# Optimization experiments

Hardware: AMD Instinct MI355X
Metric: run time of the kernel (lower is better)

## Reference

```python
import jax, jax.numpy as jnp
import numpy as np

N_NODES = 50000
N_EDGES = 800000
F_IN = 128
HEADS = 8
HID = 16
EDGE_DIM = 2
EPS = 1e-5
GAT_SLOPE = 0.2   # GATv2Conv default negative_slope
ACT_SLOPE = 0.01  # GATLayer alpha


def setup_inputs() -> dict:
    key = jax.random.key(0)
    ks = jax.random.split(key, 10)
    HC = HEADS * HID
    return {
        "x": jax.random.normal(ks[0], (N_NODES, F_IN), jnp.float32),
        "edge_idx": jax.random.randint(ks[1], (2, N_EDGES), 0, N_NODES, jnp.int32),
        "edge_attr": jax.random.normal(ks[2], (N_EDGES, EDGE_DIM), jnp.float32),
        "Wl": jax.random.normal(ks[3], (F_IN, HC), jnp.float32) * (1.0 / np.sqrt(F_IN)),
        "bl": jnp.zeros((HC,), jnp.float32),
        "Wr": jax.random.normal(ks[4], (F_IN, HC), jnp.float32) * (1.0 / np.sqrt(F_IN)),
        "br": jnp.zeros((HC,), jnp.float32),
        "We": jax.random.normal(ks[5], (EDGE_DIM, HC), jnp.float32) * (1.0 / np.sqrt(EDGE_DIM)),
        "be": jnp.zeros((HC,), jnp.float32),
        "att": jax.random.normal(ks[6], (HEADS, HID), jnp.float32) * (1.0 / np.sqrt(HID)),
        "bias": jnp.zeros((HC,), jnp.float32),
        "gamma": jnp.ones((HC,), jnp.float32),
        "beta": jnp.zeros((HC,), jnp.float32),
    }


def reference(x, edge_idx, edge_attr, Wl, bl, Wr, br, We, be, att, bias, gamma, beta):
    N = x.shape[0]
    H, C = att.shape
    # GATv2: separate source/target linear maps (share_weights=False)
    xl = (x @ Wl + bl).reshape(N, H, C)      # source transform (messages)
    xr = (x @ Wr + br).reshape(N, H, C)      # target transform
    e = (edge_attr @ We + be).reshape(-1, H, C)
    src, dst = edge_idx[0], edge_idx[1]       # edge j -> i
    # edge-wise attention input: [E, H, C]
    m = jax.nn.leaky_relu(xl[src] + xr[dst] + e, GAT_SLOPE)
    logits = jnp.einsum('ehc,hc->eh', m, att)  # [E, H]
    # segment softmax over incoming edges of each target node
    lmax = jax.ops.segment_max(logits, dst, num_segments=N)          # [N, H]
    ex = jnp.exp(logits - lmax[dst])
    denom = jax.ops.segment_sum(ex, dst, num_segments=N)             # [N, H]
    alpha = ex / denom[dst]                                          # [E, H]
    # weighted scatter-aggregate of source messages, concat heads
    out = jax.ops.segment_sum(xl[src] * alpha[:, :, None], dst, num_segments=N)
    out = out.reshape(N, H * C) + bias
    # BatchNorm over nodes (batch statistics), then LeakyReLU(0.01)
    mean = out.mean(axis=0)
    var = out.var(axis=0)
    out = (out - mean) / jnp.sqrt(var + EPS) * gamma + beta
    return jax.nn.leaky_relu(out, ACT_SLOPE)
```

## Files before the change

kernel.cpp:

```cpp
#include <hip/hip_runtime.h>
#include <hip/hip_bf16.h>

#define N_NODES 50000
#define N_EDGES 800000
#define HEADS 8
#define HID 16
#define HC 128

typedef __attribute__((ext_vector_type(8))) short bf16x8;
typedef __attribute__((ext_vector_type(4))) float f32x4;

__device__ __forceinline__ float bf2f(unsigned short u) {
  union { unsigned int i; float f; } v;
  v.i = (unsigned int)u << 16;
  return v.f;
}
__device__ __forceinline__ unsigned short f2bf(float f) {
  __hip_bfloat16 h = __float2bfloat16(f);
  return *(unsigned short*)&h;
}

__global__ __launch_bounds__(256) void k_cvt_x(const float* __restrict__ x,
                                               unsigned short* __restrict__ xb) {
  const int i = blockIdx.x * 256 + threadIdx.x;
  const float4 a = ((const float4*)x)[(size_t)i * 2];
  const float4 b = ((const float4*)x)[(size_t)i * 2 + 1];
  union { unsigned short s[8]; uint4 v; } o;
  o.s[0] = f2bf(a.x); o.s[1] = f2bf(a.y); o.s[2] = f2bf(a.z); o.s[3] = f2bf(a.w);
  o.s[4] = f2bf(b.x); o.s[5] = f2bf(b.y); o.s[6] = f2bf(b.z); o.s[7] = f2bf(b.w);
  ((uint4*)xb)[i] = o.v;
}

__global__ __launch_bounds__(128) void k_cvt_w(const float* __restrict__ Wl,
                                               const float* __restrict__ Wr,
                                               unsigned short* __restrict__ WcatT) {
  const int n = blockIdx.x;
  const int k = threadIdx.x;
  const float* W = (n < 128) ? Wl : Wr;
  WcatT[n * 128 + k] = f2bf(W[k * HC + (n & 127)]);
}

__global__ __launch_bounds__(256) void k_gemm(
    const unsigned short* __restrict__ xb, const unsigned short* __restrict__ WcatT,
    const float* __restrict__ bl, const float* __restrict__ br,
    unsigned short* __restrict__ xl, unsigned short* __restrict__ xr) {
  __shared__ unsigned short As[128 * 136];
  const int t = threadIdx.x;
  const int m0 = blockIdx.x * 128;
  const int nt = blockIdx.y;

#pragma unroll
  for (int it = 0; it < 8; ++it) {
    const int c = t + it * 256;
    const int row = c >> 4, c8 = (c & 15) * 8;
    uint4 v = make_uint4(0, 0, 0, 0);
    if (m0 + row < N_NODES) v = *(const uint4*)(xb + (size_t)(m0 + row) * HC + c8);
    *(uint4*)(&As[row * 136 + c8]) = v;
  }
  __syncthreads();

  const int w = t >> 6, lane = t & 63;
  const int wm = w >> 1, wn = w & 1;
  const int lr = lane & 15, lk = lane >> 4;

  f32x4 acc[4][4];
#pragma unroll
  for (int i = 0; i < 4; ++i)
#pragma unroll
    for (int j = 0; j < 4; ++j) acc[i][j] = (f32x4)(0.f);

  const unsigned short* Wbase = WcatT + (size_t)(nt * 128 + wn * 64 + lr) * 128;
#pragma unroll
  for (int ks = 0; ks < 4; ++ks) {
    const int k = ks * 32 + lk * 8;
    bf16x8 bfr[4], afr[4];
#pragma unroll
    for (int ni = 0; ni < 4; ++ni)
      bfr[ni] = *(const bf16x8*)(Wbase + ni * 16 * 128 + k);
#pragma unroll
    for (int mi = 0; mi < 4; ++mi)
      afr[mi] = *(const bf16x8*)(&As[(wm * 64 + mi * 16 + lr) * 136 + k]);
#pragma unroll
    for (int mi = 0; mi < 4; ++mi)
#pragma unroll
      for (int ni = 0; ni < 4; ++ni)
        acc[mi][ni] = __builtin_amdgcn_mfma_f32_16x16x32_bf16(
            afr[mi], bfr[ni], acc[mi][ni], 0, 0, 0);
  }

  const float* bvec = nt ? br : bl;
  unsigned short* __restrict__ dst = nt ? xr : xl;
#pragma unroll
  for (int ni = 0; ni < 4; ++ni) {
    const int gcol = wn * 64 + ni * 16 + lr;
    const float bb = bvec[gcol];
#pragma unroll
    for (int mi = 0; mi < 4; ++mi) {
#pragma unroll
      for (int r = 0; r < 4; ++r) {
        const int grow = m0 + wm * 64 + mi * 16 + lk * 4 + r;
        if (grow < N_NODES)
          dst[(size_t)grow * HC + gcol] = f2bf(acc[mi][ni][r] + bb);
      }
    }
  }
}

__global__ __launch_bounds__(256) void k_deg(const int* __restrict__ eidx,
                                             int* __restrict__ deg) {
  const int e = blockIdx.x * 256 + threadIdx.x;
  if (e < N_EDGES) atomicAdd(&deg[eidx[N_EDGES + e]], 1);
}

__global__ __launch_bounds__(256) void k_alloc(const int* __restrict__ deg,
                                               int* __restrict__ counter,
                                               int* __restrict__ offs) {
  const int node = blockIdx.x * 256 + threadIdx.x;
  const int lane = threadIdx.x & 63;
  const int v = (node < N_NODES) ? deg[node] : 0;
  int incl = v;
#pragma unroll
  for (int d = 1; d < 64; d <<= 1) {
    const int t = __shfl_up(incl, d);
    if (lane >= d) incl += t;
  }
  const int total = __shfl(incl, 63);
  int base = 0;
  if (lane == 63) base = atomicAdd(counter, total);
  base = __shfl(base, 63);
  if (node < N_NODES) offs[node] = base + incl - v;
}

__global__ __launch_bounds__(256) void k_scatter(
    const int* __restrict__ eidx, const float* __restrict__ eattr,
    const int* __restrict__ offs, int* __restrict__ cursor,
    int4* __restrict__ epack) {
  const int e = blockIdx.x * 256 + threadIdx.x;
  if (e < N_EDGES) {
    const int src = eidx[e];
    const int d = eidx[N_EDGES + e];
    const float2 ea = *(const float2*)(eattr + (size_t)e * 2);
    const int pos = atomicAdd(&cursor[d], 1);
    epack[offs[d] + pos] =
        make_int4(src, __float_as_int(ea.x), __float_as_int(ea.y), 0);
  }
}

__global__ __launch_bounds__(256) void k_attagg(
    const int* __restrict__ offs, const int* __restrict__ deg,
    const int4* __restrict__ epack,
    const unsigned short* __restrict__ xl, const unsigned short* __restrict__ xr,
    const float* __restrict__ We, const float* __restrict__ be,
    const float* __restrict__ att, float* __restrict__ outp) {
  const int wave = threadIdx.x >> 6, lane = threadIdx.x & 63;
  const int node = blockIdx.x * 4 + wave;
  const int c0 = lane * 2;

  const float w0a = We[c0],      w0b = We[c0 + 1];
  const float w1a = We[HC + c0], w1b = We[HC + c0 + 1];
  const float bea = be[c0],      beb = be[c0 + 1];
  const float ata = att[c0],     atb = att[c0 + 1];

  const unsigned int xrw = *((const unsigned int*)(xr + (size_t)node * HC) + lane);
  const float xra = bf2f((unsigned short)xrw);
  const float xrb = bf2f((unsigned short)(xrw >> 16));

  const int beg = offs[node];
  const int end = beg + deg[node];
  float dn = 0.f, a0 = 0.f, a1 = 0.f;

  if (beg < end) {
    const int endm1 = end - 1;
    const int nb = (end - beg + 3) >> 2;
    int4 ep0[4], ep1[4];
    unsigned int xw0[4];
#pragma unroll
    for (int j = 0; j < 4; ++j) {
      int kk = beg + j; kk = kk < endm1 ? kk : endm1;
      ep0[j] = epack[kk];
    }
#pragma unroll
    for (int j = 0; j < 4; ++j)
      xw0[j] = *((const unsigned int*)(xl + (size_t)ep0[j].x * HC) + lane);
    if (nb > 1) {
#pragma unroll
      for (int j = 0; j < 4; ++j) {
        int kk = beg + 4 + j; kk = kk < endm1 ? kk : endm1;
        ep1[j] = epack[kk];
      }
    }
    for (int b = 0; b < nb; ++b) {
      unsigned int xw1[4];
      int4 ep2[4];
      if (b + 1 < nb) {
#pragma unroll
        for (int j = 0; j < 4; ++j)
          xw1[j] = *((const unsigned int*)(xl + (size_t)ep1[j].x * HC) + lane);
      }
      if (b + 2 < nb) {
#pragma unroll
        for (int j = 0; j < 4; ++j) {
          int kk = beg + (b + 2) * 4 + j; kk = kk < endm1 ? kk : endm1;
          ep2[j] = epack[kk];
        }
      }
      const int k0 = beg + b * 4;
#pragma unroll
      for (int j = 0; j < 4; ++j) {
        const float eax = __int_as_float(ep0[j].y);
        const float eay = __int_as_float(ep0[j].z);
        const float x0 = bf2f((unsigned short)xw0[j]);
        const float x1 = bf2f((unsigned short)(xw0[j] >> 16));
        float m0 = x0 + xra + fmaf(eax, w0a, fmaf(eay, w1a, bea));
        float m1 = x1 + xrb + fmaf(eax, w0b, fmaf(eay, w1b, beb));
        m0 = m0 > 0.f ? m0 : 0.2f * m0;
        m1 = m1 > 0.f ? m1 : 0.2f * m1;
        float p = fmaf(m0, ata, m1 * atb);
        p += __shfl_xor(p, 1);
        p += __shfl_xor(p, 2);
        p += __shfl_xor(p, 4);
        const float exv = (k0 + j < end) ? __expf(p) : 0.f;
        dn += exv;
        a0 = fmaf(exv, x0, a0);
        a1 = fmaf(exv, x1, a1);
      }
#pragma unroll
      for (int j = 0; j < 4; ++j) { ep0[j] = ep1[j]; xw0[j] = xw1[j]; ep1[j] = ep2[j]; }
    }
  }
  const float inv = dn > 0.f ? 1.0f / dn : 0.f;
  float2 o;
  o.x = a0 * inv;
  o.y = a1 * inv;
  *((float2*)(outp + (size_t)node * HC) + lane) = o;
}

__global__ __launch_bounds__(256) void k_stats(const float* __restrict__ outp,
                                               float* __restrict__ stats) {
  const int c = threadIdx.x & 127;
  const int half = threadIdx.x >> 7;
  float s1 = 0.f, s2 = 0.f;
  for (int r = blockIdx.x * 2 + half; r < N_NODES; r += gridDim.x * 2) {
    const float v = outp[(size_t)r * HC + c];
    s1 += v;
    s2 = fmaf(v, v, s2);
  }
  __shared__ float sm[512];
  sm[threadIdx.x] = s1;
  sm[256 + threadIdx.x] = s2;
  __syncthreads();
  if (threadIdx.x < 128) {
    s1 = sm[threadIdx.x] + sm[threadIdx.x + 128];
    s2 = sm[256 + threadIdx.x] + sm[256 + threadIdx.x + 128];
    atomicAdd(&stats[c], s1);
    atomicAdd(&stats[128 + c], s2);
  }
}

__global__ __launch_bounds__(256) void k_bn(const float* __restrict__ stats,
                                            const float* __restrict__ gamma,
                                            const float* __restrict__ beta,
                                            float* __restrict__ outp) {
  const int i = blockIdx.x * 256 + threadIdx.x;
  if (i >= N_NODES * HC) return;
  const int c = i & 127;
  const float mean = stats[c] * (1.0f / N_NODES);
  const float var = stats[128 + c] * (1.0f / N_NODES) - mean * mean;
  const float rstd = rsqrtf(var + 1e-5f);
  float v = (outp[i] - mean) * rstd * gamma[c] + beta[c];
  outp[i] = v > 0.f ? v : 0.01f * v;
}

extern "C" void kernel_launch(void* const* d_in, const int* in_sizes, int n_in,
                              void* d_out, int out_size, void* d_ws, size_t ws_size,
                              hipStream_t stream) {
  const float* x     = (const float*)d_in[0];
  const int*   eidx  = (const int*)d_in[1];
  const float* eattr = (const float*)d_in[2];
  const float* Wl    = (const float*)d_in[3];
  const float* bl    = (const float*)d_in[4];
  const float* Wr    = (const float*)d_in[5];
  const float* br    = (const float*)d_in[6];
  const float* We    = (const float*)d_in[7];
  const float* be    = (const float*)d_in[8];
  const float* att   = (const float*)d_in[9];
  const float* gamma = (const float*)d_in[11];
  const float* beta  = (const float*)d_in[12];
  float* out = (float*)d_out;

  char* ws = (char*)d_ws;
  size_t off = 0;
  auto alloc = [&](size_t bytes) {
    size_t o = off;
    off = (off + bytes + 15) & ~size_t(15);
    return o;
  };
  const size_t o_deg   = alloc((size_t)(N_NODES + 1) * 4);
  const size_t o_cur   = alloc((size_t)N_NODES * 4);
  const size_t o_cnt   = alloc(16);
  const size_t o_stats = alloc(256 * 4);
  const size_t zero_bytes = off;
  const size_t o_offs = alloc((size_t)(N_NODES + 1) * 4);
  const size_t o_ep   = alloc((size_t)N_EDGES * 16);
  const size_t o_xb   = alloc((size_t)N_NODES * HC * 2);
  const size_t o_wt   = alloc((size_t)256 * 128 * 2);
  const size_t o_xl   = alloc((size_t)N_NODES * HC * 2);
  const size_t o_xr   = alloc((size_t)N_NODES * HC * 2);
  (void)ws_size; (void)in_sizes; (void)n_in; (void)out_size;

  int*   deg   = (int*)(ws + o_deg);
  int*   cur   = (int*)(ws + o_cur);
  int*   cnt   = (int*)(ws + o_cnt);
  float* stats = (float*)(ws + o_stats);
  int*   offs  = (int*)(ws + o_offs);
  int4*  epack = (int4*)(ws + o_ep);
  unsigned short* xb    = (unsigned short*)(ws + o_xb);
  unsigned short* WcatT = (unsigned short*)(ws + o_wt);
  unsigned short* xl    = (unsigned short*)(ws + o_xl);
  unsigned short* xr    = (unsigned short*)(ws + o_xr);

  hipMemsetAsync(ws, 0, zero_bytes, stream);

  k_cvt_x<<<3125, 256, 0, stream>>>(x, xb);
  k_cvt_w<<<256, 128, 0, stream>>>(Wl, Wr, WcatT);
  k_gemm<<<dim3(391, 2), 256, 0, stream>>>(xb, WcatT, bl, br, xl, xr);
  k_deg<<<3125, 256, 0, stream>>>(eidx, deg);
  k_alloc<<<196, 256, 0, stream>>>(deg, cnt, offs);
  k_scatter<<<3125, 256, 0, stream>>>(eidx, eattr, offs, cur, epack);
  k_attagg<<<12500, 256, 0, stream>>>(offs, deg, epack, xl, xr, We, be, att, out);
  k_stats<<<256, 256, 0, stream>>>(out, stats);
  k_bn<<<25000, 256, 0, stream>>>(stats, gamma, beta, out);
}
```

Measured before the change: 346.9 us.

## Fuse prep kernels, fold x conversion into GEMM, fuse BN stats into aggregation

Merges the degree count and weight transpose into one launch. The x-to-bf16 conversion moves into a single GEMM launch that computes both xl and xr per tile, and the offset allocation runs as extra blocks of that same launch. BatchNorm statistics are accumulated inside the attention/aggregation kernel into 8 bucketed atomics, which removes a separate stats pass over the output. The BN apply is vectorised with precomputed scale and shift, and the edge loop drops its clamped tail handling in favour of a separate remainder loop. Together these cut launches and full-tensor passes, at the cost of more atomics and more shared-memory work per aggregation block.

```diff
diff --git a/kernel.cpp b/kernel.cpp
--- a/kernel.cpp
+++ b/kernel.cpp
@@ -20,47 +20,73 @@
   return *(unsigned short*)&h;
 }
 
-__global__ __launch_bounds__(256) void k_cvt_x(const float* __restrict__ x,
-                                               unsigned short* __restrict__ xb) {
-  const int i = blockIdx.x * 256 + threadIdx.x;
-  const float4 a = ((const float4*)x)[(size_t)i * 2];
-  const float4 b = ((const float4*)x)[(size_t)i * 2 + 1];
-  union { unsigned short s[8]; uint4 v; } o;
-  o.s[0] = f2bf(a.x); o.s[1] = f2bf(a.y); o.s[2] = f2bf(a.z); o.s[3] = f2bf(a.w);
-  o.s[4] = f2bf(b.x); o.s[5] = f2bf(b.y); o.s[6] = f2bf(b.z); o.s[7] = f2bf(b.w);
-  ((uint4*)xb)[i] = o.v;
-}
-
-__global__ __launch_bounds__(128) void k_cvt_w(const float* __restrict__ Wl,
-                                               const float* __restrict__ Wr,
-                                               unsigned short* __restrict__ WcatT) {
-  const int n = blockIdx.x;
-  const int k = threadIdx.x;
-  const float* W = (n < 128) ? Wl : Wr;
-  WcatT[n * 128 + k] = f2bf(W[k * HC + (n & 127)]);
-}
-
-__global__ __launch_bounds__(256) void k_gemm(
-    const unsigned short* __restrict__ xb, const unsigned short* __restrict__ WcatT,
+__global__ __launch_bounds__(256) void k_prep(
+    const int* __restrict__ eidx, const float* __restrict__ Wl,
+    const float* __restrict__ Wr, int* __restrict__ deg,
+    unsigned short* __restrict__ WcatT) {
+  const int b = blockIdx.x;
+  if (b < 3125) {
+    const int e = b * 256 + threadIdx.x;
+    atomicAdd(&deg[eidx[N_EDGES + e]], 1);
+  } else {
+    const int idx = (b - 3125) * 256 + threadIdx.x;
+    const int n = idx >> 7, k = idx & 127;
+    const float* W = (n < 128) ? Wl : Wr;
+    WcatT[idx] = f2bf(W[k * HC + (n & 127)]);
+  }
+}
+
+__global__ __launch_bounds__(512) void k_gemm_alloc(
+    const float* __restrict__ x, const unsigned short* __restrict__ WcatT,
     const float* __restrict__ bl, const float* __restrict__ br,
-    unsigned short* __restrict__ xl, unsigned short* __restrict__ xr) {
+    unsigned short* __restrict__ xl, unsigned short* __restrict__ xr,
+    const int* __restrict__ deg, int* __restrict__ counter,
+    int* __restrict__ offs) {
   __shared__ unsigned short As[128 * 136];
   const int t = threadIdx.x;
+
+  if (blockIdx.x >= 391) {
+    const int node = (blockIdx.x - 391) * 512 + t;
+    const int lane = t & 63;
+    const int v = (node < N_NODES) ? deg[node] : 0;
+    int incl = v;
+#pragma unroll
+    for (int d = 1; d < 64; d <<= 1) {
+      const int tt = __shfl_up(incl, d);
+      if (lane >= d) incl += tt;
+    }
+    const int total = __shfl(incl, 63);
+    int base = 0;
+    if (lane == 63) base = atomicAdd(counter, total);
+    base = __shfl(base, 63);
+    if (node < N_NODES) offs[node] = base + incl - v;
+    return;
+  }
+
   const int m0 = blockIdx.x * 128;
-  const int nt = blockIdx.y;
-
-#pragma unroll
-  for (int it = 0; it < 8; ++it) {
-    const int c = t + it * 256;
-    const int row = c >> 4, c8 = (c & 15) * 8;
-    uint4 v = make_uint4(0, 0, 0, 0);
-    if (m0 + row < N_NODES) v = *(const uint4*)(xb + (size_t)(m0 + row) * HC + c8);
-    *(uint4*)(&As[row * 136 + c8]) = v;
+#pragma unroll
+  for (int it = 0; it < 4; ++it) {
+    const int c = t + it * 512;
+    const int row = c >> 4;
+    const int seg = (c & 15) * 8;
+    const int grow = m0 + row;
+    float4 a = make_float4(0.f, 0.f, 0.f, 0.f), bb2 = a;
+    if (grow < N_NODES) {
+      const float4* p = (const float4*)(x + (size_t)grow * 128 + seg);
+      a = p[0];
+      bb2 = p[1];
+    }
+    union { unsigned short s[8]; uint4 v; } o;
+    o.s[0] = f2bf(a.x);   o.s[1] = f2bf(a.y);
+    o.s[2] = f2bf(a.z);   o.s[3] = f2bf(a.w);
+    o.s[4] = f2bf(bb2.x); o.s[5] = f2bf(bb2.y);
+    o.s[6] = f2bf(bb2.z); o.s[7] = f2bf(bb2.w);
+    *(uint4*)(&As[row * 136 + seg]) = o.v;
   }
   __syncthreads();
 
   const int w = t >> 6, lane = t & 63;
-  const int wm = w >> 1, wn = w & 1;
+  const int wm = w >> 2, wn = w & 3;
   const int lr = lane & 15, lk = lane >> 4;
 
   f32x4 acc[4][4];
@@ -69,7 +95,7 @@
 #pragma unroll
     for (int j = 0; j < 4; ++j) acc[i][j] = (f32x4)(0.f);
 
-  const unsigned short* Wbase = WcatT + (size_t)(nt * 128 + wn * 64 + lr) * 128;
+  const unsigned short* Wbase = WcatT + (size_t)(wn * 64 + lr) * 128;
 #pragma unroll
   for (int ks = 0; ks < 4; ++ks) {
     const int k = ks * 32 + lk * 8;
@@ -88,47 +114,22 @@
             afr[mi], bfr[ni], acc[mi][ni], 0, 0, 0);
   }
 
-  const float* bvec = nt ? br : bl;
-  unsigned short* __restrict__ dst = nt ? xr : xl;
 #pragma unroll
   for (int ni = 0; ni < 4; ++ni) {
     const int gcol = wn * 64 + ni * 16 + lr;
-    const float bb = bvec[gcol];
+    const bool left = gcol < 128;
+    const float bb = left ? bl[gcol] : br[gcol - 128];
+    unsigned short* __restrict__ dst = left ? xl : xr;
+    const int cc = gcol & 127;
 #pragma unroll
     for (int mi = 0; mi < 4; ++mi) {
 #pragma unroll
       for (int r = 0; r < 4; ++r) {
         const int grow = m0 + wm * 64 + mi * 16 + lk * 4 + r;
-        if (grow < N_NODES)
-          dst[(size_t)grow * HC + gcol] = f2bf(acc[mi][ni][r] + bb);
+        if (grow < N_NODES) dst[(size_t)grow * HC + cc] = f2bf(acc[mi][ni][r] + bb);
       }
     }
   }
-}
-
-__global__ __launch_bounds__(256) void k_deg(const int* __restrict__ eidx,
-                                             int* __restrict__ deg) {
-  const int e = blockIdx.x * 256 + threadIdx.x;
-  if (e < N_EDGES) atomicAdd(&deg[eidx[N_EDGES + e]], 1);
-}
-
-__global__ __launch_bounds__(256) void k_alloc(const int* __restrict__ deg,
-                                               int* __restrict__ counter,
-                                               int* __restrict__ offs) {
-  const int node = blockIdx.x * 256 + threadIdx.x;
-  const int lane = threadIdx.x & 63;
-  const int v = (node < N_NODES) ? deg[node] : 0;
-  int incl = v;
-#pragma unroll
-  for (int d = 1; d < 64; d <<= 1) {
-    const int t = __shfl_up(incl, d);
-    if (lane >= d) incl += t;
-  }
-  const int total = __shfl(incl, 63);
-  int base = 0;
-  if (lane == 63) base = atomicAdd(counter, total);
-  base = __shfl(base, 63);
-  if (node < N_NODES) offs[node] = base + incl - v;
 }
 
 __global__ __launch_bounds__(256) void k_scatter(
@@ -136,139 +137,146 @@
     const int* __restrict__ offs, int* __restrict__ cursor,
     int4* __restrict__ epack) {
   const int e = blockIdx.x * 256 + threadIdx.x;
-  if (e < N_EDGES) {
-    const int src = eidx[e];
-    const int d = eidx[N_EDGES + e];
-    const float2 ea = *(const float2*)(eattr + (size_t)e * 2);
-    const int pos = atomicAdd(&cursor[d], 1);
-    epack[offs[d] + pos] =
-        make_int4(src, __float_as_int(ea.x), __float_as_int(ea.y), 0);
-  }
-}
+  const int src = eidx[e];
+  const int d = eidx[N_EDGES + e];
+  const float2 ea = *(const float2*)(eattr + (size_t)e * 2);
+  const int pos = atomicAdd(&cursor[d], 1);
+  epack[offs[d] + pos] = make_int4(src, __float_as_int(ea.x), __float_as_int(ea.y), 0);
+}
+
+#define LOADB(EP, K)                                   \
+  _Pragma("unroll") for (int j = 0; j < 4; ++j) EP[j] = epack[(K) + j];
+#define LOADX(XW, EP)                                  \
+  _Pragma("unroll") for (int j = 0; j < 4; ++j)        \
+      XW[j] = *((const unsigned int*)(xl + (size_t)EP[j].x * HC) + lane);
+#define EDGE1(EPJ, XWJ)                                                     \
+  {                                                                         \
+    const float eax = __int_as_float((EPJ).y);                              \
+    const float eay = __int_as_float((EPJ).z);                              \
+    const float x0 = bf2f((unsigned short)(XWJ));                           \
+    const float x1 = bf2f((unsigned short)((XWJ) >> 16));                   \
+    float m0 = fmaf(eax, w0a, fmaf(eay, w1a, ca)) + x0;                     \
+    float m1 = fmaf(eax, w0b, fmaf(eay, w1b, cb)) + x1;                     \
+    m0 = fmaxf(m0, 0.2f * m0);                                              \
+    m1 = fmaxf(m1, 0.2f * m1);                                              \
+    float p = fmaf(m0, ata, m1 * atb);                                      \
+    p += __shfl_xor(p, 1);                                                  \
+    p += __shfl_xor(p, 2);                                                  \
+    p += __shfl_xor(p, 4);                                                  \
+    const float exv = __expf(p);                                            \
+    dn += exv;                                                              \
+    a0 = fmaf(exv, x0, a0);                                                 \
+    a1 = fmaf(exv, x1, a1);                                                 \
+  }
+#define COMPUTE4(EP, XW)                               \
+  _Pragma("unroll") for (int j = 0; j < 4; ++j) EDGE1(EP[j], XW[j])
 
 __global__ __launch_bounds__(256) void k_attagg(
     const int* __restrict__ offs, const int* __restrict__ deg,
     const int4* __restrict__ epack,
     const unsigned short* __restrict__ xl, const unsigned short* __restrict__ xr,
     const float* __restrict__ We, const float* __restrict__ be,
-    const float* __restrict__ att, float* __restrict__ outp) {
+    const float* __restrict__ att, float* __restrict__ outp,
+    float* __restrict__ statsB) {
+  __shared__ float ssum[4 * 128];
+  __shared__ float ssq[4 * 128];
   const int wave = threadIdx.x >> 6, lane = threadIdx.x & 63;
   const int node = blockIdx.x * 4 + wave;
   const int c0 = lane * 2;
 
   const float w0a = We[c0],      w0b = We[c0 + 1];
   const float w1a = We[HC + c0], w1b = We[HC + c0 + 1];
-  const float bea = be[c0],      beb = be[c0 + 1];
   const float ata = att[c0],     atb = att[c0 + 1];
 
   const unsigned int xrw = *((const unsigned int*)(xr + (size_t)node * HC) + lane);
-  const float xra = bf2f((unsigned short)xrw);
-  const float xrb = bf2f((unsigned short)(xrw >> 16));
+  const float ca = be[c0] + bf2f((unsigned short)xrw);
+  const float cb = be[c0 + 1] + bf2f((unsigned short)(xrw >> 16));
 
   const int beg = offs[node];
-  const int end = beg + deg[node];
+  const int dn_e = deg[node];
+  const int end = beg + dn_e;
+  const int nf = dn_e >> 2;
+
   float dn = 0.f, a0 = 0.f, a1 = 0.f;
 
-  if (beg < end) {
-    const int endm1 = end - 1;
-    const int nb = (end - beg + 3) >> 2;
-    int4 ep0[4], ep1[4];
-    unsigned int xw0[4];
-#pragma unroll
-    for (int j = 0; j < 4; ++j) {
-      int kk = beg + j; kk = kk < endm1 ? kk : endm1;
-      ep0[j] = epack[kk];
-    }
-#pragma unroll
-    for (int j = 0; j < 4; ++j)
-      xw0[j] = *((const unsigned int*)(xl + (size_t)ep0[j].x * HC) + lane);
-    if (nb > 1) {
-#pragma unroll
-      for (int j = 0; j < 4; ++j) {
-        int kk = beg + 4 + j; kk = kk < endm1 ? kk : endm1;
-        ep1[j] = epack[kk];
-      }
-    }
-    for (int b = 0; b < nb; ++b) {
-      unsigned int xw1[4];
-      int4 ep2[4];
-      if (b + 1 < nb) {
-#pragma unroll
-        for (int j = 0; j < 4; ++j)
-          xw1[j] = *((const unsigned int*)(xl + (size_t)ep1[j].x * HC) + lane);
-      }
-      if (b + 2 < nb) {
-#pragma unroll
-        for (int j = 0; j < 4; ++j) {
-          int kk = beg + (b + 2) * 4 + j; kk = kk < endm1 ? kk : endm1;
-          ep2[j] = epack[kk];
-        }
-      }
-      const int k0 = beg + b * 4;
-#pragma unroll
-      for (int j = 0; j < 4; ++j) {
-        const float eax = __int_as_float(ep0[j].y);
-        const float eay = __int_as_float(ep0[j].z);
-        const float x0 = bf2f((unsigned short)xw0[j]);
-        const float x1 = bf2f((unsigned short)(xw0[j] >> 16));
-        float m0 = x0 + xra + fmaf(eax, w0a, fmaf(eay, w1a, bea));
-        float m1 = x1 + xrb + fmaf(eax, w0b, fmaf(eay, w1b, beb));
-        m0 = m0 > 0.f ? m0 : 0.2f * m0;
-        m1 = m1 > 0.f ? m1 : 0.2f * m1;
-        float p = fmaf(m0, ata, m1 * atb);
-        p += __shfl_xor(p, 1);
-        p += __shfl_xor(p, 2);
-        p += __shfl_xor(p, 4);
-        const float exv = (k0 + j < end) ? __expf(p) : 0.f;
-        dn += exv;
-        a0 = fmaf(exv, x0, a0);
-        a1 = fmaf(exv, x1, a1);
-      }
-#pragma unroll
-      for (int j = 0; j < 4; ++j) { ep0[j] = ep1[j]; xw0[j] = xw1[j]; ep1[j] = ep2[j]; }
-    }
-  }
+  if (nf >= 1) {
+    int4 epA[4], epB[4];
+    unsigned int xwA[4];
+    LOADB(epA, beg)
+    LOADX(xwA, epA)
+    if (nf >= 2) LOADB(epB, beg + 4)
+    for (int b = 0; b + 1 < nf; ++b) {
+      unsigned int xwB[4];
+      int4 epC[4];
+      LOADX(xwB, epB)
+      if (b + 2 < nf) LOADB(epC, beg + (b + 2) * 4)
+      COMPUTE4(epA, xwA)
+#pragma unroll
+      for (int j = 0; j < 4; ++j) { epA[j] = epB[j]; xwA[j] = xwB[j]; epB[j] = epC[j]; }
+    }
+    COMPUTE4(epA, xwA)
+  }
+  for (int k = beg + (nf << 2); k < end; ++k) {
+    const int4 ep = epack[k];
+    const unsigned int xw = *((const unsigned int*)(xl + (size_t)ep.x * HC) + lane);
+    EDGE1(ep, xw)
+  }
+
   const float inv = dn > 0.f ? 1.0f / dn : 0.f;
+  const float o0 = a0 * inv, o1 = a1 * inv;
   float2 o;
-  o.x = a0 * inv;
-  o.y = a1 * inv;
+  o.x = o0;
+  o.y = o1;
   *((float2*)(outp + (size_t)node * HC) + lane) = o;
-}
-
-__global__ __launch_bounds__(256) void k_stats(const float* __restrict__ outp,
-                                               float* __restrict__ stats) {
-  const int c = threadIdx.x & 127;
-  const int half = threadIdx.x >> 7;
-  float s1 = 0.f, s2 = 0.f;
-  for (int r = blockIdx.x * 2 + half; r < N_NODES; r += gridDim.x * 2) {
-    const float v = outp[(size_t)r * HC + c];
-    s1 += v;
-    s2 = fmaf(v, v, s2);
-  }
-  __shared__ float sm[512];
-  sm[threadIdx.x] = s1;
-  sm[256 + threadIdx.x] = s2;
+
+  ssum[wave * 128 + c0]     = o0;
+  ssum[wave * 128 + c0 + 1] = o1;
+  ssq[wave * 128 + c0]      = o0 * o0;
+  ssq[wave * 128 + c0 + 1]  = o1 * o1;
   __syncthreads();
   if (threadIdx.x < 128) {
-    s1 = sm[threadIdx.x] + sm[threadIdx.x + 128];
-    s2 = sm[256 + threadIdx.x] + sm[256 + threadIdx.x + 128];
-    atomicAdd(&stats[c], s1);
-    atomicAdd(&stats[128 + c], s2);
-  }
-}
-
-__global__ __launch_bounds__(256) void k_bn(const float* __restrict__ stats,
+    const int c = threadIdx.x;
+    const float s1 = ssum[c] + ssum[128 + c] + ssum[256 + c] + ssum[384 + c];
+    const float s2 = ssq[c] + ssq[128 + c] + ssq[256 + c] + ssq[384 + c];
+    float* bkt = statsB + (blockIdx.x & 7) * 256;
+    atomicAdd(&bkt[c], s1);
+    atomicAdd(&bkt[128 + c], s2);
+  }
+}
+
+__global__ __launch_bounds__(256) void k_bn(const float* __restrict__ statsB,
                                             const float* __restrict__ gamma,
                                             const float* __restrict__ beta,
                                             float* __restrict__ outp) {
-  const int i = blockIdx.x * 256 + threadIdx.x;
-  if (i >= N_NODES * HC) return;
-  const int c = i & 127;
-  const float mean = stats[c] * (1.0f / N_NODES);
-  const float var = stats[128 + c] * (1.0f / N_NODES) - mean * mean;
-  const float rstd = rsqrtf(var + 1e-5f);
-  float v = (outp[i] - mean) * rstd * gamma[c] + beta[c];
-  outp[i] = v > 0.f ? v : 0.01f * v;
+  __shared__ float sscale[128], sshift[128];
+  const int t = threadIdx.x;
+  if (t < 128) {
+    float s1 = 0.f, s2 = 0.f;
+#pragma unroll
+    for (int b = 0; b < 8; ++b) {
+      s1 += statsB[b * 256 + t];
+      s2 += statsB[b * 256 + 128 + t];
+    }
+    const float mean = s1 * (1.0f / N_NODES);
+    const float var = s2 * (1.0f / N_NODES) - mean * mean;
+    const float rstd = rsqrtf(var + 1e-5f);
+    const float sc = rstd * gamma[t];
+    sscale[t] = sc;
+    sshift[t] = beta[t] - mean * sc;
+  }
+  __syncthreads();
+  const size_t base = (size_t)blockIdx.x * 1024 + t * 4;
+  float4 v = *(const float4*)(outp + base);
+  const int c = (t * 4) & 127;
+  v.x = fmaf(v.x, sscale[c],     sshift[c]);
+  v.y = fmaf(v.y, sscale[c + 1], sshift[c + 1]);
+  v.z = fmaf(v.z, sscale[c + 2], sshift[c + 2]);
+  v.w = fmaf(v.w, sscale[c + 3], sshift[c + 3]);
+  v.x = fmaxf(v.x, 0.01f * v.x);
+  v.y = fmaxf(v.y, 0.01f * v.y);
+  v.z = fmaxf(v.z, 0.01f * v.z);
+  v.w = fmaxf(v.w, 0.01f * v.w);
+  *(float4*)(outp + base) = v;
 }
 
 extern "C" void kernel_launch(void* const* d_in, const int* in_sizes, int n_in,
@@ -298,36 +306,31 @@
   const size_t o_deg   = alloc((size_t)(N_NODES + 1) * 4);
   const size_t o_cur   = alloc((size_t)N_NODES * 4);
   const size_t o_cnt   = alloc(16);
-  const size_t o_stats = alloc(256 * 4);
+  const size_t o_stats = alloc((size_t)8 * 256 * 4);
   const size_t zero_bytes = off;
   const size_t o_offs = alloc((size_t)(N_NODES + 1) * 4);
   const size_t o_ep   = alloc((size_t)N_EDGES * 16);
-  const size_t o_xb   = alloc((size_t)N_NODES * HC * 2);
   const size_t o_wt   = alloc((size_t)256 * 128 * 2);
   const size_t o_xl   = alloc((size_t)N_NODES * HC * 2);
   const size_t o_xr   = alloc((size_t)N_NODES * HC * 2);
   (void)ws_size; (void)in_sizes; (void)n_in; (void)out_size;
 
-  int*   deg   = (int*)(ws + o_deg);
-  int*   cur   = (int*)(ws + o_cur);
-  int*   cnt   = (int*)(ws + o_cnt);
-  float* stats = (float*)(ws + o_stats);
-  int*   offs  = (int*)(ws + o_offs);
-  int4*  epack = (int4*)(ws + o_ep);
-  unsigned short* xb    = (unsigned short*)(ws + o_xb);
+  int*   deg    = (int*)(ws + o_deg);
+  int*   cur    = (int*)(ws + o_cur);
+  int*   cnt    = (int*)(ws + o_cnt);
+  float* statsB = (float*)(ws + o_stats);
+  int*   offs   = (int*)(ws + o_offs);
+  int4*  epack  = (int4*)(ws + o_ep);
   unsigned short* WcatT = (unsigned short*)(ws + o_wt);
   unsigned short* xl    = (unsigned short*)(ws + o_xl);
   unsigned short* xr    = (unsigned short*)(ws + o_xr);
 
   hipMemsetAsync(ws, 0, zero_bytes, stream);
 
-  k_cvt_x<<<3125, 256, 0, stream>>>(x, xb);
-  k_cvt_w<<<256, 128, 0, stream>>>(Wl, Wr, WcatT);
-  k_gemm<<<dim3(391, 2), 256, 0, stream>>>(xb, WcatT, bl, br, xl, xr);
-  k_deg<<<3125, 256, 0, stream>>>(eidx, deg);
-  k_alloc<<<196, 256, 0, stream>>>(deg, cnt, offs);
+  k_prep<<<3253, 256, 0, stream>>>(eidx, Wl, Wr, deg, WcatT);
+  k_gemm_alloc<<<489, 512, 0, stream>>>(x, WcatT, bl, br, xl, xr, deg, cnt, offs);
   k_scatter<<<3125, 256, 0, stream>>>(eidx, eattr, offs, cur, epack);
-  k_attagg<<<12500, 256, 0, stream>>>(offs, deg, epack, xl, xr, We, be, att, out);
-  k_stats<<<256, 256, 0, stream>>>(out, stats);
-  k_bn<<<25000, 256, 0, stream>>>(stats, gamma, beta, out);
-}
+  k_attagg<<<12500, 256, 0, stream>>>(offs, deg, epack, xl, xr, We, be, att, out,
+                                      statsB);
+  k_bn<<<6250, 256, 0, stream>>>(statsB, gamma, beta, out);
+}
```

Result: faster. 296.3 us (-14.6%).
